# Performance work log

Hardware: AMD Instinct MI355X
Metric: run time of the kernel (lower is better)

The kernel has to match this reference:

```python
import jax, jax.numpy as jnp
import numpy as np

B = 32; NPG = 500; N = B * NPG; E = 256000; F = 1024; OD = 128
DD = 80; TD = 32; NH = 4; DH = TD // NH; DFF = 128; NL = 2
LSUB = 128; MAXLEN = 4 * LSUB
NEG = -1e9; SLOPE = 0.01; EPS = 1e-5


def setup_inputs() -> dict:
    key = jax.random.key(0)
    ks = iter(jax.random.split(key, 64))
    nrm = lambda *s: jax.random.normal(next(ks), s, jnp.float32)
    w = lambda *s: nrm(*s) * 0.02
    inp = {}
    inp["pro1_x"] = nrm(N, F)
    inp["pro2_x"] = nrm(N, F)
    inp["pro1_edge_index"] = jax.random.randint(next(ks), (2, E), 0, N)
    inp["pro2_edge_index"] = jax.random.randint(next(ks), (2, E), 0, N)
    inp["pro1_batch"] = jnp.repeat(jnp.arange(B), NPG)
    inp["pro2_batch"] = jnp.repeat(jnp.arange(B), NPG)
    for nm in ("mas1_straight", "mas1_flipped", "mas2_straight", "mas2_flipped"):
        inp[nm] = nrm(B, LSUB, DD)
        inp[nm + "_lengths"] = jax.random.randint(next(ks), (B,), 1, LSUB + 1)
    inp["gcn1_w"] = w(F, F); inp["gcn1_b"] = jnp.zeros(F)
    inp["gcn2_w"] = w(F, F); inp["gcn2_b"] = jnp.zeros(F)
    inp["fc1_w"] = w(OD, F); inp["fc1_b"] = jnp.zeros(OD)
    inp["fc2_w"] = w(OD, F); inp["fc2_b"] = jnp.zeros(OD)
    inp["red_w"] = w(TD - 2, DD); inp["red_b"] = jnp.zeros(TD - 2)
    inp["attn_in_w"] = w(NL, 3 * TD, TD); inp["attn_in_b"] = jnp.zeros((NL, 3 * TD))
    inp["attn_out_w"] = w(NL, TD, TD); inp["attn_out_b"] = jnp.zeros((NL, TD))
    inp["ln1_w"] = jnp.ones((NL, TD)); inp["ln1_b"] = jnp.zeros((NL, TD))
    inp["ln2_w"] = jnp.ones((NL, TD)); inp["ln2_b"] = jnp.zeros((NL, TD))
    inp["ff1_w"] = w(NL, DFF, TD); inp["ff1_b"] = jnp.zeros((NL, DFF))
    inp["ff2_w"] = w(NL, TD, DFF); inp["ff2_b"] = jnp.zeros((NL, TD))
    inp["final_w"] = w(1, 2 * OD + TD); inp["final_b"] = jnp.zeros(1)
    return inp


def _leaky(v):
    return jnp.where(v >= 0, v, SLOPE * v)


def _gcn(x, ei, W, b):
    # GCNConv: x' = D^-1/2 (A + I) D^-1/2 (x @ W^T) + b
    sl = jnp.arange(N, dtype=ei.dtype)
    src = jnp.concatenate([ei[0], sl])
    dst = jnp.concatenate([ei[1], sl])
    deg = jax.ops.segment_sum(jnp.ones(src.shape[0], x.dtype), dst, N)
    dinv = jax.lax.rsqrt(deg)
    norm = (dinv[src] * dinv[dst])[:, None]
    h = x @ W.T
    return jax.ops.segment_sum(h[src] * norm, dst, N) + b


def _gmp(x, batch):
    # global mean pool per graph
    s = jax.ops.segment_sum(x, batch, B)
    c = jax.ops.segment_sum(jnp.ones(x.shape[0], x.dtype), batch, B)
    return s / c[:, None]


def _ln(x, w, b):
    m = x.mean(-1, keepdims=True)
    v = ((x - m) ** 2).mean(-1, keepdims=True)
    return (x - m) * jax.lax.rsqrt(v + EPS) * w + b


def _forward(pro1_x, pro1_edge_index, pro1_batch, pro2_x, pro2_edge_index, pro2_batch,
             mas1_straight, mas1_flipped, mas2_straight, mas2_flipped,
             mas1_straight_lengths, mas1_flipped_lengths, mas2_straight_lengths, mas2_flipped_lengths,
             gcn1_w, gcn1_b, fc1_w, fc1_b, gcn2_w, gcn2_b, fc2_w, fc2_b,
             red_w, red_b, attn_in_w, attn_in_b, attn_out_w, attn_out_b,
             ln1_w, ln1_b, ln2_w, ln2_b, ff1_w, ff1_b, ff2_w, ff2_b,
             final_w, final_b):
    # --- graph branches (dropout = identity at inference) ---
    x1 = _leaky(_gcn(pro1_x, pro1_edge_index, gcn1_w, gcn1_b))
    x1 = _leaky(_gmp(x1, pro1_batch) @ fc1_w.T + fc1_b)           # [B, OD]
    x2 = _leaky(_gcn(pro2_x, pro2_edge_index, gcn2_w, gcn2_b))
    x2 = _leaky(_gmp(x2, pro2_batch) @ fc2_w.T + fc2_b)           # [B, OD]

    # --- vectorized ragged pack: project, append indicators, scatter to offsets ---
    inds = ((1.0, 1.0), (0.0, 1.0), (1.0, 0.0), (0.0, 0.0))      # (straight, first)
    mas = (mas1_straight, mas1_flipped, mas2_straight, mas2_flipped)
    lens = (mas1_straight_lengths, mas1_flipped_lengths, mas2_straight_lengths, mas2_flipped_lengths)
    pos = jnp.arange(LSUB)
    brow = jnp.arange(B)[:, None]
    seq = jnp.zeros((B, MAXLEN, TD), jnp.float32)
    off = jnp.zeros((B,), lens[0].dtype)
    for m, l, (si, fi) in zip(mas, lens, inds):
        proj = m @ red_w.T + red_b                                # [B, LSUB, TD-2]
        ones = jnp.ones((B, LSUB, 1), jnp.float32)
        p = jnp.concatenate([proj, si * ones, fi * ones], -1)    # [B, LSUB, TD]
        valid = pos[None, :] < l[:, None]                        # [B, LSUB]
        idx = jnp.where(valid, off[:, None] + pos[None, :], 0)
        seq = seq.at[brow, idx].add(p * valid[..., None])
        off = off + l
    mask = jnp.arange(MAXLEN)[None, :] < off[:, None]            # [B, MAXLEN] True = valid

    # --- post-norm TransformerEncoder (relu FFN, key padding mask) ---
    x_t = seq
    for li in range(NL):
        qkv = x_t @ attn_in_w[li].T + attn_in_b[li]
        q, k, v = jnp.split(qkv, 3, axis=-1)
        q = q.reshape(B, MAXLEN, NH, DH)
        k = k.reshape(B, MAXLEN, NH, DH)
        v = v.reshape(B, MAXLEN, NH, DH)
        scores = jnp.einsum('bqhd,bkhd->bhqk', q, k) / np.float32(np.sqrt(DH))
        scores = jnp.where(mask[:, None, None, :], scores, NEG)
        attn = jax.nn.softmax(scores, axis=-1)
        o = jnp.einsum('bhqk,bkhd->bqhd', attn, v).reshape(B, MAXLEN, TD)
        o = o @ attn_out_w[li].T + attn_out_b[li]
        x_t = _ln(x_t + o, ln1_w[li], ln1_b[li])
        h = jax.nn.relu(x_t @ ff1_w[li].T + ff1_b[li]) @ ff2_w[li].T + ff2_b[li]
        x_t = _ln(x_t + h, ln2_w[li], ln2_b[li])

    mf = mask[..., None].astype(jnp.float32)
    mas_out = (x_t * mf).sum(1) / mf.sum(1)                      # masked mean [B, TD]

    combined = jnp.concatenate([x1, x2, mas_out], axis=1)        # [B, 2*OD + TD]
    return combined @ final_w.T + final_b                        # [B, 1]


def reference(pro1_x, pro1_edge_index, pro1_batch, pro2_x, pro2_edge_index, pro2_batch,
              mas1_straight, mas1_flipped, mas2_straight, mas2_flipped,
              mas1_straight_lengths, mas1_flipped_lengths, mas2_straight_lengths, mas2_flipped_lengths,
              gcn1_w, gcn1_b, fc1_w, fc1_b, gcn2_w, gcn2_b, fc2_w, fc2_b,
              red_w, red_b, attn_in_w, attn_in_b, attn_out_w, attn_out_b,
              ln1_w, ln1_b, ln2_w, ln2_b, ff1_w, ff1_b, ff2_w, ff2_b,
              final_w, final_b):
    return _forward(pro1_x, pro1_edge_index, pro1_batch, pro2_x, pro2_edge_index, pro2_batch,
                    mas1_straight, mas1_flipped, mas2_straight, mas2_flipped,
                    mas1_straight_lengths, mas1_flipped_lengths, mas2_straight_lengths, mas2_flipped_lengths,
                    gcn1_w, gcn1_b, fc1_w, fc1_b, gcn2_w, gcn2_b, fc2_w, fc2_b,
                    red_w, red_b, attn_in_w, attn_in_b, attn_out_w, attn_out_b,
                    ln1_w, ln1_b, ln2_w, ln2_b, ff1_w, ff1_b, ff2_w, ff2_b,
                    final_w, final_b)
```

## Files before the change

kernel.cpp:

```cpp
#include <hip/hip_runtime.h>
#include <stdint.h>

#define N_NODES 16000
#define B_      32
#define NPG_    500
#define E_      256000
#define F_      1024
#define OD_     128
#define DD_     80
#define TD_     32
#define NH_     4
#define DH_     8
#define DFF_    128
#define LSUB_   128
#define MAXLEN_ 512
#define EPS_    1e-5f
#define SLOPE_  0.01f

typedef __bf16 bf16x8 __attribute__((ext_vector_type(8)));
typedef float  f32x4  __attribute__((ext_vector_type(4)));

__device__ __forceinline__ float leaky(float v) { return v >= 0.f ? v : SLOPE_ * v; }

__device__ __forceinline__ unsigned short f2bf(float f) {
  unsigned u = __float_as_uint(f);
  u += 0x7FFFu + ((u >> 16) & 1u);
  return (unsigned short)(u >> 16);
}
__device__ __forceinline__ float bf2f(unsigned short u) {
  return __uint_as_float((unsigned)u << 16);
}

__device__ __forceinline__ void gld_lds16(const void* g, void* l) {
  __builtin_amdgcn_global_load_lds(
      (const __attribute__((address_space(1))) unsigned int*)g,
      (__attribute__((address_space(3))) unsigned int*)l, 16, 0, 0);
}

__global__ void k_f2bf2(const float* __restrict__ in0, const float* __restrict__ in1,
                        unsigned short* __restrict__ out0, unsigned short* __restrict__ out1,
                        int n4) {
  const float* in = blockIdx.y ? in1 : in0;
  unsigned short* out = blockIdx.y ? out1 : out0;
  int i = blockIdx.x * blockDim.x + threadIdx.x;
  int stride = gridDim.x * blockDim.x;
  for (; i < n4; i += stride) {
    float4 v = ((const float4*)in)[i];
    ushort4 o;
    o.x = f2bf(v.x); o.y = f2bf(v.y); o.z = f2bf(v.z); o.w = f2bf(v.w);
    ((ushort4*)out)[i] = o;
  }
}

__global__ __launch_bounds__(256) void k_gemm_bf16(const unsigned short* __restrict__ A,
                                                   const unsigned short* __restrict__ Bw,
                                                   unsigned short* __restrict__ C) {
  const int K = 1024, N = 1024;
  const size_t g = blockIdx.z;
  A  += g * (size_t)N_NODES * K;
  Bw += g * (size_t)K * N;
  C  += g * (size_t)N_NODES * N;
  __shared__ short As[128 * 32];
  __shared__ short Bs[128 * 32];
  const int t    = threadIdx.x;
  const int lane = t & 63, wave = t >> 6;
  const int wrow = wave >> 1, wcol = wave & 1;
  const int quad = lane >> 4, l15 = lane & 15;
  const int mBase = blockIdx.x * 128;
  const int nBase = blockIdx.y * 128;

  f32x4 acc[4][4];
  f32x4 zero = {0.f, 0.f, 0.f, 0.f};
#pragma unroll
  for (int i = 0; i < 4; ++i)
#pragma unroll
    for (int j = 0; j < 4; ++j) acc[i][j] = zero;

  const int r4 = t >> 2;
  const int c4 = (t & 3) * 8;

  for (int kt = 0; kt < 32; ++kt) {
    const int k0 = kt * 32;
    gld_lds16(&A[(size_t)(mBase + r4) * K + k0 + c4],       &As[t * 8]);
    gld_lds16(&A[(size_t)(mBase + 64 + r4) * K + k0 + c4],  &As[2048 + t * 8]);
    gld_lds16(&Bw[(size_t)(nBase + r4) * K + k0 + c4],      &Bs[t * 8]);
    gld_lds16(&Bw[(size_t)(nBase + 64 + r4) * K + k0 + c4], &Bs[2048 + t * 8]);
    __syncthreads();

    bf16x8 a[4], b[4];
#pragma unroll
    for (int ti = 0; ti < 4; ++ti)
      a[ti] = *(const bf16x8*)&As[(wrow * 64 + ti * 16 + l15) * 32 + quad * 8];
#pragma unroll
    for (int tj = 0; tj < 4; ++tj)
      b[tj] = *(const bf16x8*)&Bs[(wcol * 64 + tj * 16 + l15) * 32 + quad * 8];
#pragma unroll
    for (int ti = 0; ti < 4; ++ti)
#pragma unroll
      for (int tj = 0; tj < 4; ++tj)
        acc[ti][tj] = __builtin_amdgcn_mfma_f32_16x16x32_bf16(a[ti], b[tj], acc[ti][tj], 0, 0, 0);
    __syncthreads();
  }

#pragma unroll
  for (int ti = 0; ti < 4; ++ti)
#pragma unroll
    for (int tj = 0; tj < 4; ++tj)
#pragma unroll
      for (int r = 0; r < 4; ++r) {
        int grow = mBase + wrow * 64 + ti * 16 + quad * 4 + r;
        int gcol = nBase + wcol * 64 + tj * 16 + l15;
        C[(size_t)grow * N + gcol] = f2bf(acc[ti][tj][r]);
      }
}

__global__ void k_hist(const int* __restrict__ ei0, const int* __restrict__ ei1,
                       int* __restrict__ cnt, int e, int n) {
  const int g = blockIdx.y;
  const int* dst = (g ? ei1 : ei0) + e;
  int i = blockIdx.x * 256 + threadIdx.x;
  if (i < e) atomicAdd(&cnt[g * n + dst[i]], 1);
}

__global__ void k_scan(const int* __restrict__ cnt_all, int* __restrict__ rowstart_all,
                       int* __restrict__ cursor_all, float* __restrict__ dinv_all, int n) {
  const int g = blockIdx.x;
  const int* cnt = cnt_all + g * n;
  int* rowstart = rowstart_all + g * (n + 1);
  int* cursor   = cursor_all + g * n;
  float* dinv   = dinv_all + g * n;
  __shared__ int part[256];
  __shared__ int base[257];
  int t = threadIdx.x;
  int chunk = (n + 255) >> 8;
  int s = 0;
  for (int j = 0; j < chunk; ++j) {
    int idx = t * chunk + j;
    if (idx < n) s += cnt[idx];
  }
  part[t] = s;
  __syncthreads();
  if (t == 0) {
    int a = 0;
    for (int i = 0; i < 256; ++i) { base[i] = a; a += part[i]; }
    base[256] = a;
  }
  __syncthreads();
  int a = base[t];
  for (int j = 0; j < chunk; ++j) {
    int idx = t * chunk + j;
    if (idx < n) {
      int c = cnt[idx];
      rowstart[idx] = a; cursor[idx] = a; a += c;
      dinv[idx] = rsqrtf((float)c + 1.0f);
    }
  }
  if (t == 0) rowstart[n] = base[256];
}

__global__ void k_scatter(const int* __restrict__ ei0, const int* __restrict__ ei1,
                          const float* __restrict__ dinv_all, int* __restrict__ cursor_all,
                          int* __restrict__ csr_all, float* __restrict__ csrw_all,
                          int e, int n) {
  const int g = blockIdx.y;
  const int* ei = g ? ei1 : ei0;
  int i = blockIdx.x * 256 + threadIdx.x;
  if (i < e) {
    int s = ei[i], d = ei[e + i];
    int p = atomicAdd(&cursor_all[g * n + d], 1);
    csr_all[(size_t)g * e + p]  = s;
    csrw_all[(size_t)g * e + p] = dinv_all[g * n + s] * dinv_all[g * n + d];
  }
}

__global__ __launch_bounds__(64) void k_gather(const ushort2* __restrict__ h2,
                                               const float* __restrict__ dinv,
                                               const int* __restrict__ rowstart,
                                               const int* __restrict__ csr,
                                               const float* __restrict__ csrw,
                                               ushort2* __restrict__ agg2) {
  const int sl = blockIdx.x;
  const int i  = blockIdx.y;
  const int t  = threadIdx.x;
  __shared__ int   ssrc[64];
  __shared__ float sw[64];
  const float di = dinv[i];
  const size_t fo = (size_t)sl * 64 + t;
  ushort2 sv = h2[(size_t)i * 512 + fo];
  const float selfw = di * di;
  float ax = bf2f(sv.x) * selfw, ay = bf2f(sv.y) * selfw;
  const int beg = rowstart[i], end = rowstart[i + 1];
  for (int base = beg; base < end; base += 64) {
    int c = end - base; if (c > 64) c = 64;
    __syncthreads();
    if (t < c) { ssrc[t] = csr[base + t]; sw[t] = csrw[base + t]; }
    __syncthreads();
    int j = 0;
    for (; j + 4 <= c; j += 4) {
      ushort2 v0 = h2[(size_t)ssrc[j]     * 512 + fo];
      ushort2 v1 = h2[(size_t)ssrc[j + 1] * 512 + fo];
      ushort2 v2 = h2[(size_t)ssrc[j + 2] * 512 + fo];
      ushort2 v3 = h2[(size_t)ssrc[j + 3] * 512 + fo];
      float w0 = sw[j], w1 = sw[j + 1], w2 = sw[j + 2], w3 = sw[j + 3];
      ax += bf2f(v0.x) * w0 + bf2f(v1.x) * w1 + bf2f(v2.x) * w2 + bf2f(v3.x) * w3;
      ay += bf2f(v0.y) * w0 + bf2f(v1.y) * w1 + bf2f(v2.y) * w2 + bf2f(v3.y) * w3;
    }
    for (; j < c; ++j) {
      ushort2 v0 = h2[(size_t)ssrc[j] * 512 + fo];
      float w0 = sw[j];
      ax += bf2f(v0.x) * w0; ay += bf2f(v0.y) * w0;
    }
  }
  ushort2 o; o.x = f2bf(ax); o.y = f2bf(ay);
  agg2[(size_t)i * 512 + fo] = o;
}

__global__ void k_pool(const unsigned short* __restrict__ agg_all,
                       const float* __restrict__ bias0, const float* __restrict__ bias1,
                       float* __restrict__ pooled_all) {
  int f = blockIdx.x * 256 + threadIdx.x;
  int z = blockIdx.z;
  int g = z >> 5, b = z & 31;
  const unsigned short* agg = agg_all + (size_t)g * N_NODES * F_;
  const float* bias = g ? bias1 : bias0;
  float* pooled = pooled_all + (size_t)g * B_ * F_;
  int r0 = blockIdx.y * 100;
  float bf = bias[f];
  float s = 0.f;
  for (int r = 0; r < 100; ++r)
    s += leaky(bf2f(agg[(size_t)(b * NPG_ + r0 + r) * F_ + f]) + bf);
  atomicAdd(&pooled[b * F_ + f], s);
}

__global__ void k_fc(const float* __restrict__ pooled_all,
                     const float* __restrict__ w0, const float* __restrict__ w1,
                     const float* __restrict__ bias0, const float* __restrict__ bias1,
                     float* __restrict__ out0, float* __restrict__ out1) {
  int b = blockIdx.x, o = threadIdx.x, g = blockIdx.y;
  const float* p  = pooled_all + (size_t)g * B_ * F_ + b * F_;
  const float* wr = (g ? w1 : w0) + o * F_;
  const float* bias = g ? bias1 : bias0;
  float* out = g ? out1 : out0;
  float acc = 0.f;
  for (int f = 0; f < F_; ++f) acc += p[f] * wr[f];
  out[b * OD_ + o] = leaky(acc * (1.f / 500.f) + bias[o]);
}

__global__ void k_pack(const float* __restrict__ m0, const float* __restrict__ m1,
                       const float* __restrict__ m2, const float* __restrict__ m3,
                       const int* __restrict__ l0, const int* __restrict__ l1,
                       const int* __restrict__ l2, const int* __restrict__ l3,
                       const float* __restrict__ rw, const float* __restrict__ rb,
                       float* __restrict__ seq) {
  __shared__ float xs[DD_];
  const int p = blockIdx.x, b = blockIdx.y, k = blockIdx.z;
  const float* mas = (k == 0) ? m0 : (k == 1) ? m1 : (k == 2) ? m2 : m3;
  const int*   lk  = (k == 0) ? l0 : (k == 1) ? l1 : (k == 2) ? l2 : l3;
  const int len = lk[b];
  if (p >= len) return;
  int off = 0;
  if (k > 0) off += l0[b];
  if (k > 1) off += l1[b];
  if (k > 2) off += l2[b];
  const int t = threadIdx.x;
  for (int d = t; d < DD_; d += 64) xs[d] = mas[(size_t)(b * LSUB_ + p) * DD_ + d];
  __syncthreads();
  if (t < TD_) {
    float v;
    if (t < TD_ - 2) {
      float a = rb[t];
      const float* w = &rw[t * DD_];
      for (int d = 0; d < DD_; ++d) a += xs[d] * w[d];
      v = a;
    } else if (t == TD_ - 2) {
      v = (k == 0 || k == 2) ? 1.f : 0.f;
    } else {
      v = (k < 2) ? 1.f : 0.f;
    }
    seq[((size_t)b * MAXLEN_ + off + p) * TD_ + t] = v;
  }
}

__global__ void k_totlen(const int* __restrict__ l0, const int* __restrict__ l1,
                         const int* __restrict__ l2, const int* __restrict__ l3,
                         int* __restrict__ tot) {
  int b = threadIdx.x;
  if (b < B_) tot[b] = l0[b] + l1[b] + l2[b] + l3[b];
}

__global__ void k_qkv(const float* __restrict__ xt, const float* __restrict__ w,
                      const float* __restrict__ bias, const int* __restrict__ tot,
                      float* __restrict__ qkv) {
  __shared__ float xs[TD_];
  const int row = blockIdx.x;
  if ((row & (MAXLEN_ - 1)) >= tot[row >> 9]) return;
  const int t = threadIdx.x;
  if (t < TD_) xs[t] = xt[(size_t)row * TD_ + t];
  __syncthreads();
  if (t < 3 * TD_) {
    float a = bias[t];
    const float* wr = &w[t * TD_];
#pragma unroll
    for (int k = 0; k < TD_; ++k) a += xs[k] * wr[k];
    qkv[(size_t)row * 96 + t] = a;
  }
}

__global__ __launch_bounds__(128) void k_attn(const float* __restrict__ qkv,
                                              const int* __restrict__ tot,
                                              float* __restrict__ obuf) {
  __shared__ float Kl[MAXLEN_ * DH_];
  __shared__ float Vl[MAXLEN_ * DH_];
  const int h = blockIdx.x, b = blockIdx.y, qz = blockIdx.z;
  const int t = threadIdx.x;
  const int L = tot[b];
  if (qz * 64 >= L) return;
  const float* base = &qkv[(size_t)b * MAXLEN_ * 96];
  for (int i = t; i < L * DH_; i += 128) {
    int p = i >> 3, d = i & 7;
    Kl[i] = base[p * 96 + 32 + h * 8 + d];
    Vl[i] = base[p * 96 + 64 + h * 8 + d];
  }
  __syncthreads();
  const int qi = qz * 64 + (t >> 1);
  if (qi >= L) return;
  const int half = t & 1;
  const float scale = 0.35355339059327373f;
  float q[8];
#pragma unroll
  for (int d = 0; d < 8; ++d) q[d] = base[qi * 96 + h * 8 + d] * scale;

  float l0 = 0.f, l1 = 0.f;
  float a0[8] = {0, 0, 0, 0, 0, 0, 0, 0};
  float a1[8] = {0, 0, 0, 0, 0, 0, 0, 0};
  int j = half;
  for (; j + 2 < L; j += 4) {
    const float* kr0 = &Kl[j * 8];
    const float* kr1 = &Kl[(j + 2) * 8];
    float s0 = 0.f, s1 = 0.f;
#pragma unroll
    for (int d = 0; d < 8; ++d) { s0 += q[d] * kr0[d]; s1 += q[d] * kr1[d]; }
    float p0 = __expf(s0), p1 = __expf(s1);
    l0 += p0; l1 += p1;
    const float* vr0 = &Vl[j * 8];
    const float* vr1 = &Vl[(j + 2) * 8];
#pragma unroll
    for (int d = 0; d < 8; ++d) { a0[d] += p0 * vr0[d]; a1[d] += p1 * vr1[d]; }
  }
  for (; j < L; j += 2) {
    const float* kr = &Kl[j * 8];
    float s = 0.f;
#pragma unroll
    for (int d = 0; d < 8; ++d) s += q[d] * kr[d];
    float p = __expf(s);
    l0 += p;
    const float* vr = &Vl[j * 8];
#pragma unroll
    for (int d = 0; d < 8; ++d) a0[d] += p * vr[d];
  }
  float l = l0 + l1;
#pragma unroll
  for (int d = 0; d < 8; ++d) a0[d] += a1[d];
  l += __shfl_xor(l, 1);
#pragma unroll
  for (int d = 0; d < 8; ++d) a0[d] += __shfl_xor(a0[d], 1);
  float inv = 1.f / l;
  const int dbase = half * 4;
  float4 o;
  o.x = a0[dbase + 0] * inv; o.y = a0[dbase + 1] * inv;
  o.z = a0[dbase + 2] * inv; o.w = a0[dbase + 3] * inv;
  *(float4*)&obuf[((size_t)b * MAXLEN_ + qi) * TD_ + h * 8 + dbase] = o;
}

__global__ void k_oproj_ln(const float* __restrict__ obuf, const float* __restrict__ w,
                           const float* __restrict__ bias, const float* __restrict__ lw,
                           const float* __restrict__ lb, const int* __restrict__ tot,
                           float* __restrict__ xt) {
  const int t = threadIdx.x;
  const int r = blockIdx.x * 8 + (t >> 5);
  if ((r & (MAXLEN_ - 1)) >= tot[r >> 9]) return;
  const int j = t & 31;
  const float* orow = &obuf[(size_t)r * TD_];
  float a = bias[j] + xt[(size_t)r * TD_ + j];
  const float* wr = &w[j * TD_];
#pragma unroll
  for (int k = 0; k < TD_; ++k) a += orow[k] * wr[k];
  float s1 = a, s2 = a * a;
#pragma unroll
  for (int m = 1; m < 32; m <<= 1) {
    s1 += __shfl_xor(s1, m, 32);
    s2 += __shfl_xor(s2, m, 32);
  }
  float mean = s1 * (1.f / 32.f);
  float var  = s2 * (1.f / 32.f) - mean * mean;
  xt[(size_t)r * TD_ + j] = (a - mean) * rsqrtf(var + EPS_) * lw[j] + lb[j];
}

__global__ void k_ffn_ln(const float* __restrict__ w1, const float* __restrict__ b1,
                         const float* __restrict__ w2, const float* __restrict__ b2,
                         const float* __restrict__ lw, const float* __restrict__ lb,
                         const int* __restrict__ tot, float* __restrict__ xt) {
  const int r = blockIdx.x, t = threadIdx.x;
  if ((r & (MAXLEN_ - 1)) >= tot[r >> 9]) return;
  __shared__ float xs[TD_];
  __shared__ float hb[DFF_];
  if (t < TD_) xs[t] = xt[(size_t)r * TD_ + t];
  __syncthreads();
  {
    float a = b1[t];
    const float* wr = &w1[t * TD_];
#pragma unroll
    for (int k = 0; k < TD_; ++k) a += xs[k] * wr[k];
    hb[t] = fmaxf(a, 0.f);
  }
  __syncthreads();
  if (t < TD_) {
    float a = b2[t] + xs[t];
    const float* wr = &w2[t * DFF_];
#pragma unroll
    for (int k = 0; k < DFF_; ++k) a += hb[k] * wr[k];
    float s1 = a, s2 = a * a;
#pragma unroll
    for (int m = 1; m < 32; m <<= 1) {
      s1 += __shfl_xor(s1, m, 32);
      s2 += __shfl_xor(s2, m, 32);
    }
    float mean = s1 * (1.f / 32.f);
    float var  = s2 * (1.f / 32.f) - mean * mean;
    xt[(size_t)r * TD_ + t] = (a - mean) * rsqrtf(var + EPS_) * lw[t] + lb[t];
  }
}

__global__ void k_maskmean(const float* __restrict__ xt, const int* __restrict__ tot,
                           float* __restrict__ mout) {
  __shared__ float sbuf[8][32];
  const int b = blockIdx.x, t = threadIdx.x;
  const int j = t & 31, c = t >> 5;
  const int L = tot[b];
  float s = 0.f;
  for (int p = c; p < L; p += 8) s += xt[((size_t)b * MAXLEN_ + p) * TD_ + j];
  sbuf[c][j] = s;
  __syncthreads();
  if (t < 32) {
    float a = 0.f;
#pragma unroll
    for (int cc = 0; cc < 8; ++cc) a += sbuf[cc][t];
    mout[b * TD_ + t] = a / (float)L;
  }
}

__global__ void k_final(const float* __restrict__ x1, const float* __restrict__ x2,
                        const float* __restrict__ mo, const float* __restrict__ fw,
                        const float* __restrict__ fb, float* __restrict__ out) {
  const int b = blockIdx.x, t = threadIdx.x;
  float s = 0.f;
  for (int i = t; i < 2 * OD_ + TD_; i += 64) {
    float c = (i < OD_) ? x1[b * OD_ + i]
            : (i < 2 * OD_) ? x2[b * OD_ + (i - OD_)]
            : mo[b * TD_ + (i - 2 * OD_)];
    s += fw[i] * c;
  }
#pragma unroll
  for (int m = 1; m < 64; m <<= 1) s += __shfl_xor(s, m, 64);
  if (t == 0) out[b] = s + fb[0];
}

extern "C" void kernel_launch(void* const* d_in, const int* in_sizes, int n_in,
                              void* d_out, int out_size, void* d_ws, size_t ws_size,
                              hipStream_t stream) {
  (void)in_sizes; (void)n_in; (void)out_size; (void)ws_size;
  const float* pro_x[2]  = {(const float*)d_in[0], (const float*)d_in[1]};
  const int*   pro_ei[2] = {(const int*)d_in[2], (const int*)d_in[3]};
  const float* mas[4]    = {(const float*)d_in[6], (const float*)d_in[8],
                            (const float*)d_in[10], (const float*)d_in[12]};
  const int*   lens[4]   = {(const int*)d_in[7], (const int*)d_in[9],
                            (const int*)d_in[11], (const int*)d_in[13]};
  const float* gw[2]  = {(const float*)d_in[14], (const float*)d_in[16]};
  const float* gb[2]  = {(const float*)d_in[15], (const float*)d_in[17]};
  const float* fcw[2] = {(const float*)d_in[18], (const float*)d_in[20]};
  const float* fcb[2] = {(const float*)d_in[19], (const float*)d_in[21]};
  const float* red_w = (const float*)d_in[22];
  const float* red_b = (const float*)d_in[23];
  const float* attn_in_w  = (const float*)d_in[24];
  const float* attn_in_b  = (const float*)d_in[25];
  const float* attn_out_w = (const float*)d_in[26];
  const float* attn_out_b = (const float*)d_in[27];
  const float* ln1_w = (const float*)d_in[28];
  const float* ln1_b = (const float*)d_in[29];
  const float* ln2_w = (const float*)d_in[30];
  const float* ln2_b = (const float*)d_in[31];
  const float* ff1_w = (const float*)d_in[32];
  const float* ff1_b = (const float*)d_in[33];
  const float* ff2_w = (const float*)d_in[34];
  const float* ff2_b = (const float*)d_in[35];
  const float* final_w = (const float*)d_in[36];
  const float* final_b = (const float*)d_in[37];
  float* out = (float*)d_out;

  char* p = (char*)d_ws;
  auto carve = [&](size_t bytes) -> void* {
    void* r = (void*)p;
    p += (bytes + 255) & ~(size_t)255;
    return r;
  };
  unsigned short* xb  = (unsigned short*)carve((size_t)2 * N_NODES * F_ * 2);
  unsigned short* Wb  = (unsigned short*)carve((size_t)2 * F_ * F_ * 2);
  unsigned short* h   = (unsigned short*)carve((size_t)2 * N_NODES * F_ * 2);
  unsigned short* agg = (unsigned short*)carve((size_t)2 * N_NODES * F_ * 2);
  int*   cnt      = (int*)carve((size_t)2 * N_NODES * 4);
  float* dinv     = (float*)carve((size_t)2 * N_NODES * 4);
  int*   rowstart = (int*)carve((size_t)2 * (N_NODES + 1) * 4);
  int*   cursor   = (int*)carve((size_t)2 * N_NODES * 4);
  int*   csr      = (int*)carve((size_t)2 * E_ * 4);
  float* csrw     = (float*)carve((size_t)2 * E_ * 4);
  float* pooled   = (float*)carve((size_t)2 * B_ * F_ * 4);
  float* xg[2];
  xg[0] = (float*)carve((size_t)B_ * OD_ * 4);
  xg[1] = (float*)carve((size_t)B_ * OD_ * 4);
  float* seq    = (float*)carve((size_t)B_ * MAXLEN_ * TD_ * 4);
  float* qkv    = (float*)carve((size_t)B_ * MAXLEN_ * 96 * 4);
  float* obuf   = (float*)carve((size_t)B_ * MAXLEN_ * TD_ * 4);
  int*   totlen = (int*)carve((size_t)B_ * 4);
  float* masout = (float*)carve((size_t)B_ * TD_ * 4);

  k_f2bf2<<<dim3(1024, 2), 256, 0, stream>>>(pro_x[0], pro_x[1], xb,
                                             xb + (size_t)N_NODES * F_, (N_NODES * F_) / 4);
  k_f2bf2<<<dim3(512, 2), 256, 0, stream>>>(gw[0], gw[1], Wb, Wb + (size_t)F_ * F_,
                                            (F_ * F_) / 4);
  k_gemm_bf16<<<dim3(125, 8, 2), 256, 0, stream>>>(xb, Wb, h);
  hipMemsetAsync(cnt, 0, (size_t)2 * N_NODES * 4, stream);
  k_hist<<<dim3(1000, 2), 256, 0, stream>>>(pro_ei[0], pro_ei[1], cnt, E_, N_NODES);
  k_scan<<<2, 256, 0, stream>>>(cnt, rowstart, cursor, dinv, N_NODES);
  k_scatter<<<dim3(1000, 2), 256, 0, stream>>>(pro_ei[0], pro_ei[1], dinv, cursor,
                                               csr, csrw, E_, N_NODES);
  for (int g = 0; g < 2; ++g) {
    k_gather<<<dim3(8, N_NODES), 64, 0, stream>>>(
        (const ushort2*)(h + (size_t)g * N_NODES * F_), dinv + (size_t)g * N_NODES,
        rowstart + (size_t)g * (N_NODES + 1), csr + (size_t)g * E_, csrw + (size_t)g * E_,
        (ushort2*)(agg + (size_t)g * N_NODES * F_));
  }
  hipMemsetAsync(pooled, 0, (size_t)2 * B_ * F_ * 4, stream);
  k_pool<<<dim3(4, 5, 64), 256, 0, stream>>>(agg, gb[0], gb[1], pooled);
  k_fc<<<dim3(B_, 2), 128, 0, stream>>>(pooled, fcw[0], fcw[1], fcb[0], fcb[1],
                                        xg[0], xg[1]);

  hipMemsetAsync(seq, 0, (size_t)B_ * MAXLEN_ * TD_ * 4, stream);
  k_pack<<<dim3(LSUB_, B_, 4), 64, 0, stream>>>(mas[0], mas[1], mas[2], mas[3],
                                                lens[0], lens[1], lens[2], lens[3],
                                                red_w, red_b, seq);
  k_totlen<<<1, 64, 0, stream>>>(lens[0], lens[1], lens[2], lens[3], totlen);

  for (int li = 0; li < 2; ++li) {
    k_qkv<<<B_ * MAXLEN_, 128, 0, stream>>>(seq, attn_in_w + (size_t)li * 96 * TD_,
                                            attn_in_b + (size_t)li * 96, totlen, qkv);
    k_attn<<<dim3(NH_, B_, 8), 128, 0, stream>>>(qkv, totlen, obuf);
    k_oproj_ln<<<(B_ * MAXLEN_) / 8, 256, 0, stream>>>(
        obuf, attn_out_w + (size_t)li * TD_ * TD_, attn_out_b + (size_t)li * TD_,
        ln1_w + (size_t)li * TD_, ln1_b + (size_t)li * TD_, totlen, seq);
    k_ffn_ln<<<B_ * MAXLEN_, 128, 0, stream>>>(
        ff1_w + (size_t)li * DFF_ * TD_, ff1_b + (size_t)li * DFF_,
        ff2_w + (size_t)li * TD_ * DFF_, ff2_b + (size_t)li * TD_,
        ln2_w + (size_t)li * TD_, ln2_b + (size_t)li * TD_, totlen, seq);
  }

  k_maskmean<<<B_, 256, 0, stream>>>(seq, totlen, masout);
  k_final<<<B_, 64, 0, stream>>>(xg[0], xg[1], masout, final_w, final_b, out);
}
```

Measured before the change: 815.0 us.

## Remap GEMM blocks for XCD-aware L2 reuse and restructure LDS tile layout

The GEMM launch becomes a flat 1D grid. Block ids are remapped so that consecutive blocks, which round-robin across the XCDs, share A row tiles within the same XCD's L2. The LDS layout is changed to 16-row subtiles stored in MFMA fragment order, which should reduce bank conflicts on the ds_read of fragments. The grid is padded to 128 M-tiles, so some blocks exit early, and the mapping assumes an 8-XCD round-robin dispatch.

```diff
diff --git a/kernel.cpp b/kernel.cpp
--- a/kernel.cpp
+++ b/kernel.cpp
@@ -56,44 +56,55 @@
                                                    const unsigned short* __restrict__ Bw,
                                                    unsigned short* __restrict__ C) {
   const int K = 1024, N = 1024;
-  const size_t g = blockIdx.z;
-  A  += g * (size_t)N_NODES * K;
-  Bw += g * (size_t)K * N;
-  C  += g * (size_t)N_NODES * N;
-  __shared__ short As[128 * 32];
-  __shared__ short Bs[128 * 32];
+  const int id = blockIdx.x;
+  const int g  = id >> 10;
+  const int l  = id & 1023;
+  const int xcd = l & 7;
+  const int j   = l >> 3;
+  const int mIdx = xcd + 8 * (j >> 3);
+  const int nIdx = j & 7;
+  if (mIdx >= 125) return;
+  A  += (size_t)g * N_NODES * K;
+  Bw += (size_t)g * K * N;
+  C  += (size_t)g * N_NODES * N;
+  const int mBase = mIdx * 128;
+  const int nBase = nIdx * 128;
+
+  __shared__ short As[8 * 512];
+  __shared__ short Bs[8 * 512];
   const int t    = threadIdx.x;
   const int lane = t & 63, wave = t >> 6;
   const int wrow = wave >> 1, wcol = wave & 1;
   const int quad = lane >> 4, l15 = lane & 15;
-  const int mBase = blockIdx.x * 128;
-  const int nBase = blockIdx.y * 128;
+  const int rI = lane & 15;
+  const int cI = lane >> 4;
 
   f32x4 acc[4][4];
   f32x4 zero = {0.f, 0.f, 0.f, 0.f};
 #pragma unroll
   for (int i = 0; i < 4; ++i)
 #pragma unroll
-    for (int j = 0; j < 4; ++j) acc[i][j] = zero;
-
-  const int r4 = t >> 2;
-  const int c4 = (t & 3) * 8;
+    for (int jj = 0; jj < 4; ++jj) acc[i][jj] = zero;
 
   for (int kt = 0; kt < 32; ++kt) {
     const int k0 = kt * 32;
-    gld_lds16(&A[(size_t)(mBase + r4) * K + k0 + c4],       &As[t * 8]);
-    gld_lds16(&A[(size_t)(mBase + 64 + r4) * K + k0 + c4],  &As[2048 + t * 8]);
-    gld_lds16(&Bw[(size_t)(nBase + r4) * K + k0 + c4],      &Bs[t * 8]);
-    gld_lds16(&Bw[(size_t)(nBase + 64 + r4) * K + k0 + c4], &Bs[2048 + t * 8]);
+#pragma unroll
+    for (int jj = 0; jj < 2; ++jj) {
+      const int tile = wave * 2 + jj;
+      gld_lds16(&A[(size_t)(mBase + tile * 16 + rI) * K + k0 + cI * 8],
+                &As[tile * 512 + lane * 8]);
+      gld_lds16(&Bw[(size_t)(nBase + tile * 16 + rI) * K + k0 + cI * 8],
+                &Bs[tile * 512 + lane * 8]);
+    }
     __syncthreads();
 
     bf16x8 a[4], b[4];
 #pragma unroll
     for (int ti = 0; ti < 4; ++ti)
-      a[ti] = *(const bf16x8*)&As[(wrow * 64 + ti * 16 + l15) * 32 + quad * 8];
+      a[ti] = *(const bf16x8*)&As[(wrow * 4 + ti) * 512 + quad * 128 + l15 * 8];
 #pragma unroll
     for (int tj = 0; tj < 4; ++tj)
-      b[tj] = *(const bf16x8*)&Bs[(wcol * 64 + tj * 16 + l15) * 32 + quad * 8];
+      b[tj] = *(const bf16x8*)&Bs[(wcol * 4 + tj) * 512 + quad * 128 + l15 * 8];
 #pragma unroll
     for (int ti = 0; ti < 4; ++ti)
 #pragma unroll
@@ -527,7 +538,7 @@
                                              xb + (size_t)N_NODES * F_, (N_NODES * F_) / 4);
   k_f2bf2<<<dim3(512, 2), 256, 0, stream>>>(gw[0], gw[1], Wb, Wb + (size_t)F_ * F_,
                                             (F_ * F_) / 4);
-  k_gemm_bf16<<<dim3(125, 8, 2), 256, 0, stream>>>(xb, Wb, h);
+  k_gemm_bf16<<<2048, 256, 0, stream>>>(xb, Wb, h);
   hipMemsetAsync(cnt, 0, (size_t)2 * N_NODES * 4, stream);
   k_hist<<<dim3(1000, 2), 256, 0, stream>>>(pro_ei[0], pro_ei[1], cnt, E_, N_NODES);
   k_scan<<<2, 256, 0, stream>>>(cnt, rowstart, cursor, dinv, N_NODES);
```

After: 844.6 us. +3.6%, slower.
